# Performance work log

Hardware: AMD Instinct MI355X
Metric: run time of the kernel (lower is better)

Reference implementation:

```python
import jax, jax.numpy as jnp
import numpy as np

EPS = 1e-15
B, N, F, K = 16, 1024, 512, 128  # graphs, max_nodes, feat dim, clusters


def setup_inputs() -> dict:
    key = jax.random.key(0)
    k0, k1, k2 = jax.random.split(key, 3)
    rng = np.random.default_rng(0)
    # Ragged graph sizes (between N/2 and N nodes per graph)
    counts = rng.integers(N // 2, N + 1, size=B)
    T = int(counts.sum())
    batch = np.repeat(np.arange(B), counts)
    starts = np.repeat(np.concatenate([[0], np.cumsum(counts)[:-1]]), counts)
    column = np.arange(T) - starts
    flat_index = batch * N + column  # as in _build_motifpool_dense_layout
    mask_flat = np.zeros(B * N, dtype=bool)
    mask_flat[flat_index] = True
    mask = mask_flat.reshape(B, N)
    x = jax.random.normal(k0, (T, F), dtype=jnp.float32)
    s = jax.random.normal(k1, (T, K), dtype=jnp.float32)
    a = jax.random.uniform(k2, (B, N, N), dtype=jnp.float32)
    m = jnp.asarray(mask)
    adj = (a + a.transpose(0, 2, 1)) * m[:, :, None] * m[:, None, :]
    return {
        'x': x,
        's': s,
        'adj': adj,
        'flat_index': jnp.asarray(flat_index, dtype=jnp.int32),
        'mask': m,
    }


def reference(x, s, adj, flat_index, mask):
    Bn, Nn = mask.shape
    Fd = x.shape[-1]
    Kd = s.shape[-1]
    # ragged -> dense scatter (index_copy_ equivalent)
    xd = jnp.zeros((Bn * Nn, Fd), x.dtype).at[flat_index].set(x).reshape(Bn, Nn, Fd)
    sd = jnp.zeros((Bn * Nn, Kd), s.dtype).at[flat_index].set(s).reshape(Bn, Nn, Kd)
    fmask = mask[..., None].astype(x.dtype)  # [B,N,1]
    sm = jax.nn.softmax(sd, axis=-1) * fmask
    xm = xd * fmask
    # pooled features and adjacency
    out = jnp.einsum('bnk,bnf->bkf', sm, xm)
    sa = jnp.einsum('bnk,bnm->bkm', sm, adj)
    out_adj = jnp.einsum('bkm,bml->bkl', sa, sm)
    # mincut loss: tr(S^T A S) / tr(S^T D S)
    mincut_num = jnp.trace(out_adj, axis1=-2, axis2=-1)
    d_flat = adj.sum(-1)  # node degrees [B,N]
    mincut_den = jnp.einsum('bn,bnk,bnk->b', d_flat, sm, sm)
    mincut_loss = jnp.mean(-(mincut_num / mincut_den))
    # orthogonality loss
    ss = jnp.einsum('bnk,bnl->bkl', sm, sm)
    ss_norm = jnp.linalg.norm(ss, axis=(-2, -1), keepdims=True)
    i_s = jnp.eye(Kd, dtype=ss.dtype)
    ortho_loss = jnp.mean(
        jnp.linalg.norm(ss / ss_norm - i_s / jnp.sqrt(jnp.asarray(Kd, ss.dtype)),
                        axis=(-2, -1)))
    # zero diagonal, symmetric degree-normalize
    eye_b = jnp.eye(Kd, dtype=bool)
    out_adj = jnp.where(eye_b, jnp.zeros((), out_adj.dtype), out_adj)
    d = jnp.sqrt(out_adj.sum(-1))[:, None, :] + EPS  # [B,1,K]
    out_adj = out_adj / d / d.transpose(0, 2, 1)
    return (sm, out, out_adj, mincut_loss, ortho_loss)
```

## Files before the change

kernel.cpp:

```cpp
#include <hip/hip_runtime.h>

constexpr int NB = 16, NN = 1024, NF = 512, NK = 128;
constexpr int NCH = 8;
constexpr int MSPLIT = 2;
constexpr float EPSV = 1e-15f;

typedef __attribute__((ext_vector_type(8))) short bf16x8;
typedef __attribute__((ext_vector_type(4))) float f32x4;

__device__ __forceinline__ f32x4 MFMA(bf16x8 a, bf16x8 b, f32x4 c) {
  return __builtin_amdgcn_mfma_f32_16x16x32_bf16(a, b, c, 0, 0, 0);
}

__device__ __forceinline__ unsigned short bf16_rn(float f) {
  unsigned int u = __float_as_uint(f);
  u += 0x7fffu + ((u >> 16) & 1u);
  return (unsigned short)(u >> 16);
}
__device__ __forceinline__ float bf16f(unsigned short h) {
  return __uint_as_float((unsigned int)h << 16);
}
__device__ __forceinline__ void split2(float f, unsigned short& h, unsigned short& lo) {
  h = bf16_rn(f);
  lo = bf16_rn(f - bf16f(h));
}

__global__ __launch_bounds__(256) void k_build_rowof(const int* __restrict__ fidx,
                                                     int* __restrict__ rowof, int T) {
  int t = blockIdx.x * 256 + threadIdx.x;
  if (t < T) rowof[fidx[t]] = t;
}

__global__ __launch_bounds__(256) void k_softmax(const float* __restrict__ s,
                                                 const int* __restrict__ rowof,
                                                 float* __restrict__ sm,
                                                 unsigned short* __restrict__ smTh,
                                                 unsigned short* __restrict__ smTl) {
  __shared__ float P[64][129];
  int blk = blockIdx.x;
  int b = blk >> 4, n0 = (blk & 15) * 64;
  int tid = threadIdx.x, wv = tid >> 6, lane = tid & 63;
  for (int i = 0; i < 16; ++i) {
    int r = wv * 16 + i;
    int ri = rowof[b * NN + n0 + r];
    float e0 = 0.f, e1 = 0.f;
    if (ri >= 0) {
      const float* row = s + (size_t)ri * NK;
      float a = row[lane], c = row[lane + 64];
      float m = fmaxf(a, c);
#pragma unroll
      for (int off = 32; off; off >>= 1) m = fmaxf(m, __shfl_xor(m, off, 64));
      e0 = expf(a - m);
      e1 = expf(c - m);
      float sum = e0 + e1;
#pragma unroll
      for (int off = 32; off; off >>= 1) sum += __shfl_xor(sum, off, 64);
      float inv = 1.0f / sum;
      e0 *= inv;
      e1 *= inv;
    }
    P[r][lane] = e0;
    P[r][lane + 64] = e1;
  }
  __syncthreads();
  int r2 = tid >> 2, cb = (tid & 3) * 32;
  float* orow = sm + ((size_t)b * NN + n0 + r2) * NK + cb;
#pragma unroll
  for (int j = 0; j < 8; ++j) {
    float4 v = make_float4(P[r2][cb + j * 4], P[r2][cb + j * 4 + 1],
                           P[r2][cb + j * 4 + 2], P[r2][cb + j * 4 + 3]);
    *(float4*)(orow + j * 4) = v;
  }
  for (int j = 0; j < 32; ++j) {
    int k = wv * 32 + j;
    float v = P[lane][k];
    unsigned short h, lo;
    split2(v, h, lo);
    size_t off = ((size_t)b * NK + k) * NN + n0 + lane;
    smTh[off] = h;
    smTl[off] = lo;
  }
}

__global__ __launch_bounds__(256) void k_adj_sm(const float* __restrict__ adj,
                                                const unsigned short* __restrict__ smTh,
                                                const unsigned short* __restrict__ smTl,
                                                float* __restrict__ Ytp,
                                                float* __restrict__ dfp) {
  __shared__ __align__(16) unsigned short STh[128][72], STl[128][72];
  __shared__ __align__(16) unsigned short ADh[64][72], ADl[64][72];
  int b = blockIdx.y, n0 = blockIdx.x * 64, z = blockIdx.z;
  int tid = threadIdx.x, wv = tid >> 6, l = tid & 63;
  int lr = l & 15, lk = l >> 4;
  int tk = tid >> 1, th = tid & 1;
  int sn = tid >> 2, sq = tid & 3;
  const float* A = adj + (size_t)b * NN * NN;
  f32x4 zero = {0.f, 0.f, 0.f, 0.f};
  f32x4 acc[2][4];
#pragma unroll
  for (int i = 0; i < 2; ++i)
#pragma unroll
    for (int j = 0; j < 4; ++j) acc[i][j] = zero;
  float rsacc = 0.f;
  for (int m0 = z * (NN / MSPLIT); m0 < (z + 1) * (NN / MSPLIT); m0 += 64) {
    __syncthreads();
    {
      const uint4* gh = (const uint4*)(smTh + ((size_t)b * NK + tk) * NN + m0 + th * 32);
      const uint4* gl = (const uint4*)(smTl + ((size_t)b * NK + tk) * NN + m0 + th * 32);
#pragma unroll
      for (int j = 0; j < 4; ++j) {
        *(uint4*)&STh[tk][th * 32 + j * 8] = gh[j];
        *(uint4*)&STl[tk][th * 32 + j * 8] = gl[j];
      }
    }
    {
      const float* ap = A + (size_t)(n0 + sn) * NN + m0 + sq * 16;
      float ps = 0.f;
#pragma unroll
      for (int j = 0; j < 4; ++j) {
        float4 v = *(const float4*)(ap + j * 4);
        ushort4 vh, vl;
        split2(v.x, vh.x, vl.x);
        split2(v.y, vh.y, vl.y);
        split2(v.z, vh.z, vl.z);
        split2(v.w, vh.w, vl.w);
        *(ushort4*)&ADh[sn][sq * 16 + j * 4] = vh;
        *(ushort4*)&ADl[sn][sq * 16 + j * 4] = vl;
        ps += v.x + v.y + v.z + v.w;
      }
      ps += __shfl_xor(ps, 1, 64);
      ps += __shfl_xor(ps, 2, 64);
      rsacc += ps;
    }
    __syncthreads();
#pragma unroll
    for (int s = 0; s < 2; ++s) {
      bf16x8 ah0 = *(const bf16x8*)&STh[wv * 32 + lr][s * 32 + lk * 8];
      bf16x8 ah1 = *(const bf16x8*)&STh[wv * 32 + 16 + lr][s * 32 + lk * 8];
      bf16x8 al0 = *(const bf16x8*)&STl[wv * 32 + lr][s * 32 + lk * 8];
      bf16x8 al1 = *(const bf16x8*)&STl[wv * 32 + 16 + lr][s * 32 + lk * 8];
#pragma unroll
      for (int nt = 0; nt < 4; ++nt) {
        bf16x8 bh = *(const bf16x8*)&ADh[nt * 16 + lr][s * 32 + lk * 8];
        bf16x8 bl = *(const bf16x8*)&ADl[nt * 16 + lr][s * 32 + lk * 8];
        acc[0][nt] = MFMA(ah0, bh, acc[0][nt]);
        acc[0][nt] = MFMA(ah0, bl, acc[0][nt]);
        acc[0][nt] = MFMA(al0, bh, acc[0][nt]);
        acc[1][nt] = MFMA(ah1, bh, acc[1][nt]);
        acc[1][nt] = MFMA(ah1, bl, acc[1][nt]);
        acc[1][nt] = MFMA(al1, bh, acc[1][nt]);
      }
    }
  }
  float* Yb = Ytp + ((size_t)z * NB + b) * NK * NN;
#pragma unroll
  for (int kt = 0; kt < 2; ++kt)
#pragma unroll
    for (int nt = 0; nt < 4; ++nt)
#pragma unroll
      for (int reg = 0; reg < 4; ++reg) {
        int k = wv * 32 + kt * 16 + lk * 4 + reg;
        int n = n0 + nt * 16 + lr;
        Yb[(size_t)k * NN + n] = acc[kt][nt][reg];
      }
  if (sq == 0) dfp[((size_t)z * NB + b) * NN + n0 + sn] = rsacc;
}

__global__ __launch_bounds__(256) void k_dflat(const float* __restrict__ dfp,
                                               float* __restrict__ dflat) {
  int i = blockIdx.x * 256 + threadIdx.x;
  dflat[i] = dfp[i] + dfp[NB * NN + i];
}

__global__ __launch_bounds__(512) void k_feat(const float* __restrict__ sm,
                                              const float* __restrict__ x,
                                              const int* __restrict__ rowof,
                                              float* __restrict__ out0,
                                              float* __restrict__ out1) {
  __shared__ float Ss[64][128];
  __shared__ float Xs[64][68];
  int b = blockIdx.y;
  int fbase = blockIdx.x * 64;
  int z = blockIdx.z;
  const float* S = sm + (size_t)b * NN * NK;
  int tid = threadIdx.x;
  int tk = tid >> 4, tf = tid & 15;
  int k0 = tk * 4, f0 = tf * 4;
  float acc[4][4] = {};
  for (int n0 = z * (NN / 2); n0 < (z + 1) * (NN / 2); n0 += 64) {
    __syncthreads();
#pragma unroll
    for (int p = 0; p < 4; ++p) {
      int r = p * 16 + (tid >> 5);
      int c = (tid & 31) * 4;
      *(float4*)&Ss[r][c] = *(const float4*)(S + (size_t)(n0 + r) * NK + c);
    }
#pragma unroll
    for (int p = 0; p < 2; ++p) {
      int r = p * 32 + (tid >> 4);
      int c = (tid & 15) * 4;
      int ri = rowof[b * NN + n0 + r];
      float4 v = make_float4(0.f, 0.f, 0.f, 0.f);
      if (ri >= 0) v = *(const float4*)(x + (size_t)ri * NF + fbase + c);
      *(float4*)&Xs[r][c] = v;
    }
    __syncthreads();
#pragma unroll
    for (int nn = 0; nn < 64; ++nn) {
      float a[4], bb[4];
      *(float4*)a = *(const float4*)&Ss[nn][k0];
      *(float4*)bb = *(const float4*)&Xs[nn][f0];
#pragma unroll
      for (int i = 0; i < 4; ++i)
#pragma unroll
        for (int j = 0; j < 4; ++j)
          acc[i][j] = fmaf(a[i], bb[j], acc[i][j]);
    }
  }
  float* O = (z ? out1 : out0) + (size_t)b * NK * NF;
#pragma unroll
  for (int i = 0; i < 4; ++i)
    *(float4*)(O + (size_t)(k0 + i) * NF + fbase + f0) = *(float4*)&acc[i][0];
}

__global__ __launch_bounds__(256) void k_red_feat(float* __restrict__ out0,
                                                  const float* __restrict__ out1) {
  size_t i = (size_t)blockIdx.x * 256 + threadIdx.x;
  float4 a = ((const float4*)out0)[i];
  float4 c = ((const float4*)out1)[i];
  a.x += c.x; a.y += c.y; a.z += c.z; a.w += c.w;
  ((float4*)out0)[i] = a;
}

__global__ __launch_bounds__(256) void k_tt(const unsigned short* __restrict__ smTh,
                                            const unsigned short* __restrict__ smTl,
                                            const float* __restrict__ Ytp,
                                            const float* __restrict__ dflat,
                                            float* __restrict__ padj,
                                            float* __restrict__ pss,
                                            float* __restrict__ denb) {
  __shared__ __align__(16) unsigned short STh[128][40], STl[128][40];
  __shared__ __align__(16) unsigned short YTh[128][40], YTl[128][40];
  __shared__ float red[256];
  int ch = blockIdx.x, b = blockIdx.y, z = blockIdx.z;
  int nbase = ch * 128;
  int tid = threadIdx.x, wv = tid >> 6, l = tid & 63;
  int lr = l & 15, lk = l >> 4;
  int tk = tid >> 1, th = tid & 1;
  f32x4 zero = {0.f, 0.f, 0.f, 0.f};
  f32x4 acc[2][8];
#pragma unroll
  for (int i = 0; i < 2; ++i)
#pragma unroll
    for (int j = 0; j < 8; ++j) acc[i][j] = zero;
  float denp = 0.f;
  for (int c = 0; c < 4; ++c) {
    int nn0 = nbase + c * 32;
    __syncthreads();
    {
      const unsigned short* gh = smTh + ((size_t)b * NK + tk) * NN + nn0 + th * 16;
      const unsigned short* gl = smTl + ((size_t)b * NK + tk) * NN + nn0 + th * 16;
#pragma unroll
      for (int j = 0; j < 4; ++j) {
        ushort4 hj = *(const ushort4*)(gh + j * 4);
        ushort4 lj = *(const ushort4*)(gl + j * 4);
        *(ushort4*)&STh[tk][th * 16 + j * 4] = hj;
        *(ushort4*)&STl[tk][th * 16 + j * 4] = lj;
        if (z) {
          float4 dv = *(const float4*)(dflat + (size_t)b * NN + nn0 + th * 16 + j * 4);
          float v0 = bf16f(hj.x) + bf16f(lj.x), v1 = bf16f(hj.y) + bf16f(lj.y);
          float v2 = bf16f(hj.z) + bf16f(lj.z), v3 = bf16f(hj.w) + bf16f(lj.w);
          denp += dv.x * v0 * v0 + dv.y * v1 * v1 + dv.z * v2 * v2 + dv.w * v3 * v3;
        }
      }
    }
    if (!z) {
      const float* y0 = Ytp + ((size_t)b * NK + tk) * NN + nn0 + th * 16;
      const float* y1 = y0 + (size_t)NB * NK * NN;
#pragma unroll
      for (int j = 0; j < 4; ++j) {
        float4 a = *(const float4*)(y0 + j * 4);
        float4 cc = *(const float4*)(y1 + j * 4);
        a.x += cc.x; a.y += cc.y; a.z += cc.z; a.w += cc.w;
        ushort4 vh, vl;
        split2(a.x, vh.x, vl.x);
        split2(a.y, vh.y, vl.y);
        split2(a.z, vh.z, vl.z);
        split2(a.w, vh.w, vl.w);
        *(ushort4*)&YTh[tk][th * 16 + j * 4] = vh;
        *(ushort4*)&YTl[tk][th * 16 + j * 4] = vl;
      }
    }
    __syncthreads();
    unsigned short(*Bh)[40] = z ? STh : YTh;
    unsigned short(*Bl)[40] = z ? STl : YTl;
    bf16x8 ah0 = *(const bf16x8*)&STh[wv * 32 + lr][lk * 8];
    bf16x8 ah1 = *(const bf16x8*)&STh[wv * 32 + 16 + lr][lk * 8];
    bf16x8 al0 = *(const bf16x8*)&STl[wv * 32 + lr][lk * 8];
    bf16x8 al1 = *(const bf16x8*)&STl[wv * 32 + 16 + lr][lk * 8];
#pragma unroll
    for (int ct = 0; ct < 8; ++ct) {
      bf16x8 bh = *(const bf16x8*)&Bh[ct * 16 + lr][lk * 8];
      bf16x8 bl = *(const bf16x8*)&Bl[ct * 16 + lr][lk * 8];
      acc[0][ct] = MFMA(ah0, bh, acc[0][ct]);
      acc[0][ct] = MFMA(ah0, bl, acc[0][ct]);
      acc[0][ct] = MFMA(al0, bh, acc[0][ct]);
      acc[1][ct] = MFMA(ah1, bh, acc[1][ct]);
      acc[1][ct] = MFMA(ah1, bl, acc[1][ct]);
      acc[1][ct] = MFMA(al1, bh, acc[1][ct]);
    }
  }
  float* O = (z ? pss : padj) + ((size_t)ch * NB + b) * NK * NK;
#pragma unroll
  for (int kt = 0; kt < 2; ++kt)
#pragma unroll
    for (int ct = 0; ct < 8; ++ct)
#pragma unroll
      for (int reg = 0; reg < 4; ++reg)
        O[(size_t)(wv * 32 + kt * 16 + lk * 4 + reg) * NK + ct * 16 + lr] =
            acc[kt][ct][reg];
  if (z) {
    red[tid] = denp;
    __syncthreads();
#pragma unroll
    for (int sft = 128; sft; sft >>= 1) {
      if (tid < sft) red[tid] += red[tid + sft];
      __syncthreads();
    }
    if (tid == 0) atomicAdd(&denb[b], red[0]);
  }
}

__global__ __launch_bounds__(256) void k_reduce(const float* __restrict__ padj,
                                                const float* __restrict__ pss,
                                                float* __restrict__ adjraw,
                                                float* __restrict__ ssb) {
  size_t i = (size_t)blockIdx.x * 256 + threadIdx.x;
  size_t stride4 = (size_t)NB * NK * NK / 4;
  const float4* pa = (const float4*)padj + i;
  const float4* ps = (const float4*)pss + i;
  float4 a = make_float4(0.f, 0.f, 0.f, 0.f);
  float4 s = make_float4(0.f, 0.f, 0.f, 0.f);
#pragma unroll
  for (int ch = 0; ch < NCH; ++ch) {
    float4 va = pa[(size_t)ch * stride4];
    float4 vs = ps[(size_t)ch * stride4];
    a.x += va.x; a.y += va.y; a.z += va.z; a.w += va.w;
    s.x += vs.x; s.y += vs.y; s.z += vs.z; s.w += vs.w;
  }
  ((float4*)adjraw)[i] = a;
  ((float4*)ssb)[i] = s;
}

__device__ __forceinline__ float block_reduce_sum(float v, float* red) {
  int tid = threadIdx.x;
  red[tid] = v;
  __syncthreads();
#pragma unroll
  for (int sft = 128; sft; sft >>= 1) {
    if (tid < sft) red[tid] += red[tid + sft];
    __syncthreads();
  }
  float r = red[0];
  __syncthreads();
  return r;
}

__global__ __launch_bounds__(256) void k_finalize(const float* __restrict__ denb,
                                                  const float* __restrict__ ssb,
                                                  float* __restrict__ out_adj,
                                                  float* __restrict__ out_loss) {
  __shared__ float red[256];
  __shared__ float sd[NK];
  int b = blockIdx.x, tid = threadIdx.x;
  float* AR = out_adj + (size_t)b * NK * NK;
  const float* SS = ssb + (size_t)b * NK * NK;

  float tv = (tid < NK) ? AR[tid * NK + tid] : 0.f;
  float trace = block_reduce_sum(tv, red);
  float den = denb[b];

  float n2 = 0.f;
  for (int i4 = tid; i4 < NK * NK / 4; i4 += 256) {
    float4 v = *(const float4*)(SS + (size_t)i4 * 4);
    n2 += v.x * v.x + v.y * v.y + v.z * v.z + v.w * v.w;
  }
  float nrm = sqrtf(block_reduce_sum(n2, red));

  const float isk = 0.08838834764831845f;
  float osum = 0.f;
  for (int i = tid; i < NK * NK; i += 256) {
    int r = i >> 7, c = i & (NK - 1);
    float val = SS[i] / nrm - ((r == c) ? isk : 0.f);
    osum += val * val;
  }
  float ortho = sqrtf(block_reduce_sum(osum, red));

  if (tid < NK) {
    float rsumv = 0.f;
    const float* row = AR + (size_t)tid * NK;
    for (int j = 0; j < NK; ++j) rsumv += (j == tid) ? 0.f : row[j];
    sd[tid] = sqrtf(rsumv) + EPSV;
  }
  __syncthreads();

  for (int i = tid; i < NK * NK; i += 256) {
    int r = i >> 7, c = i & (NK - 1);
    AR[i] = (r == c) ? 0.f : AR[i] / (sd[r] * sd[c]);
  }

  if (tid == 0) {
    atomicAdd(&out_loss[0], -(trace / den) * (1.0f / NB));
    atomicAdd(&out_loss[1], ortho * (1.0f / NB));
  }
}

extern "C" void kernel_launch(void* const* d_in, const int* in_sizes, int n_in,
                              void* d_out, int out_size, void* d_ws, size_t ws_size,
                              hipStream_t stream) {
  const float* x = (const float*)d_in[0];
  const float* s = (const float*)d_in[1];
  const float* adj = (const float*)d_in[2];
  const int* fidx = (const int*)d_in[3];
  int T = in_sizes[3];

  float* out_sm = (float*)d_out;
  float* out_feat = out_sm + (size_t)NB * NN * NK;
  float* out_adj = out_feat + (size_t)NB * NK * NF;
  float* out_loss = out_adj + (size_t)NB * NK * NK;

  float* Ytp = (float*)d_ws;
  float* dfp = Ytp + (size_t)2 * NB * NK * NN;
  float* dflat = dfp + (size_t)2 * NB * NN;
  float* padj = dflat + (size_t)NB * NN;
  float* pss = padj + (size_t)NCH * NB * NK * NK;
  float* ssb = pss + (size_t)NCH * NB * NK * NK;
  float* outf1 = ssb + (size_t)NB * NK * NK;
  float* denb = outf1 + (size_t)NB * NK * NF;
  unsigned short* smTh = (unsigned short*)(denb + 16);
  unsigned short* smTl = smTh + (size_t)NB * NK * NN;
  int* rowof = (int*)(smTl + (size_t)NB * NK * NN);

  hipMemsetAsync(out_loss, 0, 2 * sizeof(float), stream);
  hipMemsetAsync(denb, 0, 16 * sizeof(float), stream);
  hipMemsetAsync(rowof, 0xFF, (size_t)NB * NN * sizeof(int), stream);

  k_build_rowof<<<(T + 255) / 256, 256, 0, stream>>>(fidx, rowof, T);
  k_softmax<<<NB * NN / 64, 256, 0, stream>>>(s, rowof, out_sm, smTh, smTl);
  k_adj_sm<<<dim3(NN / 64, NB, MSPLIT), 256, 0, stream>>>(adj, smTh, smTl, Ytp, dfp);
  k_dflat<<<NB * NN / 256, 256, 0, stream>>>(dfp, dflat);
  k_feat<<<dim3(NF / 64, NB, 2), 512, 0, stream>>>(out_sm, x, rowof, out_feat, outf1);
  k_red_feat<<<NB * NK * NF / 4 / 256, 256, 0, stream>>>(out_feat, outf1);
  k_tt<<<dim3(NCH, NB, 2), 256, 0, stream>>>(smTh, smTl, Ytp, dflat, padj, pss, denb);
  k_reduce<<<NB * NK * NK / 4 / 256, 256, 0, stream>>>(padj, pss, out_adj, ssb);
  k_finalize<<<NB, 256, 0, stream>>>(denb, ssb, out_adj, out_loss);
}
```

Baseline: 279.6 us.

## Fuse rowof into softmax, use split-bf16 MFMA for features, drop small kernels

Builds the row index inside the softmax kernel by binary-searching the sorted flat_index, which removes the rowof memset and its scatter kernel. The feature pooling kernel switches from fp32 FMA to three-term split-bf16 MFMA using the transposed softmax buffers, and splits K across blocks so there is no partial-output reduction kernel. Degree sums are folded into k_tt, and the denominator atomics become per-chunk partials summed in finalize. Together these cut launches and scalar FMA work, at the cost of slightly lower precision in the pooled features and uncoalesced transposed LDS writes for x.

```diff
diff --git a/kernel.cpp b/kernel.cpp
--- a/kernel.cpp
+++ b/kernel.cpp
@@ -25,24 +25,32 @@
   lo = bf16_rn(f - bf16f(h));
 }
 
-__global__ __launch_bounds__(256) void k_build_rowof(const int* __restrict__ fidx,
-                                                     int* __restrict__ rowof, int T) {
-  int t = blockIdx.x * 256 + threadIdx.x;
-  if (t < T) rowof[fidx[t]] = t;
-}
-
 __global__ __launch_bounds__(256) void k_softmax(const float* __restrict__ s,
-                                                 const int* __restrict__ rowof,
+                                                 const int* __restrict__ fidx, int T,
                                                  float* __restrict__ sm,
                                                  unsigned short* __restrict__ smTh,
-                                                 unsigned short* __restrict__ smTl) {
+                                                 unsigned short* __restrict__ smTl,
+                                                 int* __restrict__ rowof) {
   __shared__ float P[64][129];
+  __shared__ int rof[64];
   int blk = blockIdx.x;
   int b = blk >> 4, n0 = (blk & 15) * 64;
   int tid = threadIdx.x, wv = tid >> 6, lane = tid & 63;
+  if (tid < 64) {
+    int d = b * NN + n0 + tid;
+    int lo = 0, hi = T;
+    while (lo < hi) {
+      int mid = (lo + hi) >> 1;
+      if (fidx[mid] < d) lo = mid + 1; else hi = mid;
+    }
+    int r = (lo < T && fidx[lo] == d) ? lo : -1;
+    rof[tid] = r;
+    rowof[d] = r;
+  }
+  __syncthreads();
   for (int i = 0; i < 16; ++i) {
     int r = wv * 16 + i;
-    int ri = rowof[b * NN + n0 + r];
+    int ri = rof[r];
     float e0 = 0.f, e1 = 0.f;
     if (ri >= 0) {
       const float* row = s + (size_t)ri * NK;
@@ -166,79 +174,81 @@
   if (sq == 0) dfp[((size_t)z * NB + b) * NN + n0 + sn] = rsacc;
 }
 
-__global__ __launch_bounds__(256) void k_dflat(const float* __restrict__ dfp,
-                                               float* __restrict__ dflat) {
-  int i = blockIdx.x * 256 + threadIdx.x;
-  dflat[i] = dfp[i] + dfp[NB * NN + i];
-}
-
-__global__ __launch_bounds__(512) void k_feat(const float* __restrict__ sm,
+__global__ __launch_bounds__(512) void k_feat(const unsigned short* __restrict__ smTh,
+                                              const unsigned short* __restrict__ smTl,
                                               const float* __restrict__ x,
                                               const int* __restrict__ rowof,
-                                              float* __restrict__ out0,
-                                              float* __restrict__ out1) {
-  __shared__ float Ss[64][128];
-  __shared__ float Xs[64][68];
-  int b = blockIdx.y;
-  int fbase = blockIdx.x * 64;
-  int z = blockIdx.z;
-  const float* S = sm + (size_t)b * NN * NK;
-  int tid = threadIdx.x;
-  int tk = tid >> 4, tf = tid & 15;
-  int k0 = tk * 4, f0 = tf * 4;
-  float acc[4][4] = {};
-  for (int n0 = z * (NN / 2); n0 < (z + 1) * (NN / 2); n0 += 64) {
-    __syncthreads();
-#pragma unroll
-    for (int p = 0; p < 4; ++p) {
-      int r = p * 16 + (tid >> 5);
-      int c = (tid & 31) * 4;
-      *(float4*)&Ss[r][c] = *(const float4*)(S + (size_t)(n0 + r) * NK + c);
-    }
-#pragma unroll
-    for (int p = 0; p < 2; ++p) {
-      int r = p * 32 + (tid >> 4);
-      int c = (tid & 15) * 4;
-      int ri = rowof[b * NN + n0 + r];
-      float4 v = make_float4(0.f, 0.f, 0.f, 0.f);
-      if (ri >= 0) v = *(const float4*)(x + (size_t)ri * NF + fbase + c);
-      *(float4*)&Xs[r][c] = v;
-    }
-    __syncthreads();
-#pragma unroll
-    for (int nn = 0; nn < 64; ++nn) {
-      float a[4], bb[4];
-      *(float4*)a = *(const float4*)&Ss[nn][k0];
-      *(float4*)bb = *(const float4*)&Xs[nn][f0];
-#pragma unroll
-      for (int i = 0; i < 4; ++i)
-#pragma unroll
-        for (int j = 0; j < 4; ++j)
-          acc[i][j] = fmaf(a[i], bb[j], acc[i][j]);
-    }
-  }
-  float* O = (z ? out1 : out0) + (size_t)b * NK * NF;
-#pragma unroll
-  for (int i = 0; i < 4; ++i)
-    *(float4*)(O + (size_t)(k0 + i) * NF + fbase + f0) = *(float4*)&acc[i][0];
-}
-
-__global__ __launch_bounds__(256) void k_red_feat(float* __restrict__ out0,
-                                                  const float* __restrict__ out1) {
-  size_t i = (size_t)blockIdx.x * 256 + threadIdx.x;
-  float4 a = ((const float4*)out0)[i];
-  float4 c = ((const float4*)out1)[i];
-  a.x += c.x; a.y += c.y; a.z += c.z; a.w += c.w;
-  ((float4*)out0)[i] = a;
+                                              float* __restrict__ outf) {
+  __shared__ __align__(16) unsigned short STh[64][72], STl[64][72];
+  __shared__ __align__(16) unsigned short XTh[64][72], XTl[64][72];
+  int b = blockIdx.y, fbase = blockIdx.x * 64, kh = blockIdx.z * 64;
+  int tid = threadIdx.x, wv = tid >> 6, l = tid & 63;
+  int lr = l & 15, lk = l >> 4;
+  int wk = (wv >> 1) * 16, wf = (wv & 1) * 32;
+  int tk = tid >> 3, tq = tid & 7;
+  f32x4 zero = {0.f, 0.f, 0.f, 0.f};
+  f32x4 acc[2] = {zero, zero};
+  for (int n0 = 0; n0 < NN; n0 += 64) {
+    __syncthreads();
+    {
+      const uint4* gh = (const uint4*)(smTh + ((size_t)b * NK + kh + tk) * NN + n0 + tq * 8);
+      const uint4* gl = (const uint4*)(smTl + ((size_t)b * NK + kh + tk) * NN + n0 + tq * 8);
+      *(uint4*)&STh[tk][tq * 8] = gh[0];
+      *(uint4*)&STl[tk][tq * 8] = gl[0];
+    }
+    {
+      int ri = rowof[b * NN + n0 + tk];
+      if (ri >= 0) {
+        const float* xp = x + (size_t)ri * NF + fbase + tq * 8;
+#pragma unroll
+        for (int j = 0; j < 2; ++j) {
+          float4 v = *(const float4*)(xp + j * 4);
+          unsigned short h, lo;
+          split2(v.x, h, lo); XTh[tq * 8 + j * 4 + 0][tk] = h; XTl[tq * 8 + j * 4 + 0][tk] = lo;
+          split2(v.y, h, lo); XTh[tq * 8 + j * 4 + 1][tk] = h; XTl[tq * 8 + j * 4 + 1][tk] = lo;
+          split2(v.z, h, lo); XTh[tq * 8 + j * 4 + 2][tk] = h; XTl[tq * 8 + j * 4 + 2][tk] = lo;
+          split2(v.w, h, lo); XTh[tq * 8 + j * 4 + 3][tk] = h; XTl[tq * 8 + j * 4 + 3][tk] = lo;
+        }
+      } else {
+#pragma unroll
+        for (int e = 0; e < 8; ++e) {
+          XTh[tq * 8 + e][tk] = 0;
+          XTl[tq * 8 + e][tk] = 0;
+        }
+      }
+    }
+    __syncthreads();
+#pragma unroll
+    for (int s = 0; s < 2; ++s) {
+      bf16x8 ah = *(const bf16x8*)&STh[wk + lr][s * 32 + lk * 8];
+      bf16x8 al = *(const bf16x8*)&STl[wk + lr][s * 32 + lk * 8];
+#pragma unroll
+      for (int ft = 0; ft < 2; ++ft) {
+        bf16x8 bh = *(const bf16x8*)&XTh[wf + ft * 16 + lr][s * 32 + lk * 8];
+        bf16x8 bl = *(const bf16x8*)&XTl[wf + ft * 16 + lr][s * 32 + lk * 8];
+        acc[ft] = MFMA(ah, bh, acc[ft]);
+        acc[ft] = MFMA(ah, bl, acc[ft]);
+        acc[ft] = MFMA(al, bh, acc[ft]);
+      }
+    }
+  }
+#pragma unroll
+  for (int ft = 0; ft < 2; ++ft)
+#pragma unroll
+    for (int reg = 0; reg < 4; ++reg) {
+      int kg = kh + wk + lk * 4 + reg;
+      int fg = fbase + wf + ft * 16 + lr;
+      outf[((size_t)b * NK + kg) * NF + fg] = acc[ft][reg];
+    }
 }
 
 __global__ __launch_bounds__(256) void k_tt(const unsigned short* __restrict__ smTh,
                                             const unsigned short* __restrict__ smTl,
                                             const float* __restrict__ Ytp,
-                                            const float* __restrict__ dflat,
+                                            const float* __restrict__ dfp,
                                             float* __restrict__ padj,
                                             float* __restrict__ pss,
-                                            float* __restrict__ denb) {
+                                            float* __restrict__ denp_arr) {
   __shared__ __align__(16) unsigned short STh[128][40], STl[128][40];
   __shared__ __align__(16) unsigned short YTh[128][40], YTl[128][40];
   __shared__ float red[256];
@@ -267,10 +277,12 @@
         *(ushort4*)&STh[tk][th * 16 + j * 4] = hj;
         *(ushort4*)&STl[tk][th * 16 + j * 4] = lj;
         if (z) {
-          float4 dv = *(const float4*)(dflat + (size_t)b * NN + nn0 + th * 16 + j * 4);
+          float4 da = *(const float4*)(dfp + (size_t)b * NN + nn0 + th * 16 + j * 4);
+          float4 db = *(const float4*)(dfp + (size_t)(NB + b) * NN + nn0 + th * 16 + j * 4);
           float v0 = bf16f(hj.x) + bf16f(lj.x), v1 = bf16f(hj.y) + bf16f(lj.y);
           float v2 = bf16f(hj.z) + bf16f(lj.z), v3 = bf16f(hj.w) + bf16f(lj.w);
-          denp += dv.x * v0 * v0 + dv.y * v1 * v1 + dv.z * v2 * v2 + dv.w * v3 * v3;
+          denp += (da.x + db.x) * v0 * v0 + (da.y + db.y) * v1 * v1 +
+                  (da.z + db.z) * v2 * v2 + (da.w + db.w) * v3 * v3;
         }
       }
     }
@@ -327,7 +339,7 @@
       if (tid < sft) red[tid] += red[tid + sft];
       __syncthreads();
     }
-    if (tid == 0) atomicAdd(&denb[b], red[0]);
+    if (tid == 0) denp_arr[ch * NB + b] = red[0];
   }
 }
 
@@ -366,7 +378,7 @@
   return r;
 }
 
-__global__ __launch_bounds__(256) void k_finalize(const float* __restrict__ denb,
+__global__ __launch_bounds__(256) void k_finalize(const float* __restrict__ denp_arr,
                                                   const float* __restrict__ ssb,
                                                   float* __restrict__ out_adj,
                                                   float* __restrict__ out_loss) {
@@ -378,7 +390,9 @@
 
   float tv = (tid < NK) ? AR[tid * NK + tid] : 0.f;
   float trace = block_reduce_sum(tv, red);
-  float den = denb[b];
+  float den = 0.f;
+#pragma unroll
+  for (int ch = 0; ch < NCH; ++ch) den += denp_arr[ch * NB + b];
 
   float n2 = 0.f;
   for (int i4 = tid; i4 < NK * NK / 4; i4 += 256) {
@@ -431,27 +445,20 @@
 
   float* Ytp = (float*)d_ws;
   float* dfp = Ytp + (size_t)2 * NB * NK * NN;
-  float* dflat = dfp + (size_t)2 * NB * NN;
-  float* padj = dflat + (size_t)NB * NN;
+  float* padj = dfp + (size_t)2 * NB * NN;
   float* pss = padj + (size_t)NCH * NB * NK * NK;
   float* ssb = pss + (size_t)NCH * NB * NK * NK;
-  float* outf1 = ssb + (size_t)NB * NK * NK;
-  float* denb = outf1 + (size_t)NB * NK * NF;
-  unsigned short* smTh = (unsigned short*)(denb + 16);
+  float* denp = ssb + (size_t)NB * NK * NK;
+  unsigned short* smTh = (unsigned short*)(denp + NCH * NB);
   unsigned short* smTl = smTh + (size_t)NB * NK * NN;
   int* rowof = (int*)(smTl + (size_t)NB * NK * NN);
 
   hipMemsetAsync(out_loss, 0, 2 * sizeof(float), stream);
-  hipMemsetAsync(denb, 0, 16 * sizeof(float), stream);
-  hipMemsetAsync(rowof, 0xFF, (size_t)NB * NN * sizeof(int), stream);
-
-  k_build_rowof<<<(T + 255) / 256, 256, 0, stream>>>(fidx, rowof, T);
-  k_softmax<<<NB * NN / 64, 256, 0, stream>>>(s, rowof, out_sm, smTh, smTl);
+
+  k_softmax<<<NB * NN / 64, 256, 0, stream>>>(s, fidx, T, out_sm, smTh, smTl, rowof);
   k_adj_sm<<<dim3(NN / 64, NB, MSPLIT), 256, 0, stream>>>(adj, smTh, smTl, Ytp, dfp);
-  k_dflat<<<NB * NN / 256, 256, 0, stream>>>(dfp, dflat);
-  k_feat<<<dim3(NF / 64, NB, 2), 512, 0, stream>>>(out_sm, x, rowof, out_feat, outf1);
-  k_red_feat<<<NB * NK * NF / 4 / 256, 256, 0, stream>>>(out_feat, outf1);
-  k_tt<<<dim3(NCH, NB, 2), 256, 0, stream>>>(smTh, smTl, Ytp, dflat, padj, pss, denb);
+  k_feat<<<dim3(NF / 64, NB, 2), 512, 0, stream>>>(smTh, smTl, x, rowof, out_feat);
+  k_tt<<<dim3(NCH, NB, 2), 256, 0, stream>>>(smTh, smTl, Ytp, dfp, padj, pss, denp);
   k_reduce<<<NB * NK * NK / 4 / 256, 256, 0, stream>>>(padj, pss, out_adj, ssb);
-  k_finalize<<<NB, 256, 0, stream>>>(denb, ssb, out_adj, out_loss);
-}
+  k_finalize<<<NB, 256, 0, stream>>>(denp, ssb, out_adj, out_loss);
+}
```

After: 253.3 us. -9.4%, faster.
